# Kernel optimization log

Measured on AMD Instinct MI355X. Metric: run time of the kernel, lower is better.

## Reference

```python
import jax, jax.numpy as jnp
import numpy as np

H = 64           # edge/node/global hidden size
IN_F = 4         # node_attr_size
OUT_F = 1        # out_size
NUM_EMB = 100    # edge_num_embeddings
SKIP = True


def setup_inputs() -> dict:
    key = jax.random.key(0)
    ks = jax.random.split(key, 24)
    T, N, E = 4, 20000, 320000
    NNZ = 340000
    inp = {
        'node_attr': jax.random.normal(ks[0], (T, N, IN_F), jnp.float32),
        'global_attr': jax.random.normal(ks[1], (1, H), jnp.float32),
        'L_values': jax.random.normal(ks[2], (NNZ,), jnp.float32),
        'coeff': jnp.ones((1,), jnp.float32),
        'edge_attr': jax.random.randint(ks[3], (T, E), 0, NUM_EMB),
        'edge_index': jax.random.randint(ks[4], (2, E), 0, N),
        'L_index': jax.random.randint(ks[5], (2, NNZ), 0, N),
        'num_processing_steps': 4,
        # parameters
        'emb': jax.random.normal(ks[6], (NUM_EMB, H), jnp.float32) * 0.05,
        'W_ne': jax.random.normal(ks[7], (IN_F, H), jnp.float32) * 0.1,
        'b_ne': jnp.zeros((H,), jnp.float32),
        'W_eb': jax.random.normal(ks[8], ((H + 2 * H) * 2 + H, H), jnp.float32) * 0.05,
        'b_eb': jnp.zeros((H,), jnp.float32),
        'W_nb': jax.random.normal(ks[9], (2 * H + 2 * H + H, H), jnp.float32) * 0.05,
        'b_nb': jnp.zeros((H,), jnp.float32),
        'W_gb': jax.random.normal(ks[10], (H + H + H, H), jnp.float32) * 0.05,
        'b_gb': jnp.zeros((H,), jnp.float32),
        'W_d1': jax.random.normal(ks[11], (H, H), jnp.float32) * 0.1,
        'b_d1': jnp.zeros((H,), jnp.float32),
        'W_d2': jax.random.normal(ks[12], (H, OUT_F), jnp.float32) * 0.1,
        'b_d2': jnp.zeros((OUT_F,), jnp.float32),
        'W_i1': jax.random.normal(ks[13], (H, H), jnp.float32) * 0.1,
        'b_i1': jnp.zeros((H,), jnp.float32),
        'W_i2': jax.random.normal(ks[14], (H, IN_F), jnp.float32) * 0.1,
        'b_i2': jnp.zeros((IN_F,), jnp.float32),
    }
    return inp


def reference(node_attr, global_attr, L_values, coeff, emb, W_ne, b_ne,
              W_eb, b_eb, W_nb, b_nb, W_gb, b_gb, W_d1, b_d1, W_d2, b_d2,
              W_i1, b_i1, W_i2, b_i2, edge_attr, edge_index, L_index,
              num_processing_steps):
    T, N, _ = node_attr.shape
    s, r = edge_index[0], edge_index[1]
    Li, Lj = L_index[0], L_index[1]

    # encoders (all T steps at once)
    x_enc = jax.nn.relu(node_attr @ W_ne + b_ne)   # [T,N,H]
    e_enc = emb[edge_attr]                         # [T,E,H]

    def laplacian(h):  # sparse sp_L @ h, h: [N,H]
        return jax.ops.segment_sum(L_values[:, None] * h[Lj], Li, num_segments=N)

    def step(carry, xe):
        h_x, h_e, h_g = carry
        x_t, e_t = xe
        node_cat = jnp.concatenate([x_t, h_x], axis=-1)          # [N,2H]
        edge_cat = jnp.concatenate([e_t, h_e], axis=-1)          # [E,2H]
        g = h_g[0]                                               # [H]
        E_ = edge_cat.shape[0]
        # EdgeBlock: edges + sender + receiver + globals
        eb_in = jnp.concatenate([edge_cat, node_cat[s], node_cat[r],
                                 jnp.broadcast_to(g, (E_, g.shape[0]))], axis=-1)
        e_new = jax.nn.relu(eb_in @ W_eb + b_eb)                 # [E,H]
        # NodeBlock: scatter_add aggregates of received/sent edges
        recv = jax.ops.segment_sum(e_new, r, num_segments=N)
        sent = jax.ops.segment_sum(e_new, s, num_segments=N)
        nb_in = jnp.concatenate([recv, sent, node_cat,
                                 jnp.broadcast_to(g, (N, g.shape[0]))], axis=-1)
        x_new = jax.nn.relu(nb_in @ W_nb + b_nb)                 # [N,H]
        # GlobalBlock: scatter_mean (single graph -> mean)
        gb_in = jnp.concatenate([e_new.mean(0), x_new.mean(0), g])[None]
        g_new = jax.nn.relu(gb_in @ W_gb + b_gb)                 # [1,H]
        h_x_next = h_x + x_new if SKIP else x_new
        time_d = h_x_next - h_x
        spat_d = coeff[0] * laplacian(h_x_next)  # pde='diff': coeff * L u
        return (h_x_next, e_new, g_new), (h_x_next, time_d, spat_d)

    h0 = (jnp.zeros((N, H), jnp.float32),
          jnp.zeros((e_enc.shape[1], H), jnp.float32),
          global_attr)
    _, (hid, time_d, spat_d) = jax.lax.scan(step, h0, (x_enc, e_enc))

    # decoders over all steps
    out_nodes = jax.nn.relu(hid @ W_d1 + b_d1) @ W_d2 + b_d2     # [T,N,OUT_F]
    pred_in = jax.nn.relu(hid @ W_i1 + b_i1) @ W_i2 + b_i2       # [T,N,IN_F]
    return out_nodes, time_d, spat_d, pred_in
```

## Files before the change

### kernel.cpp

```cpp
#include <hip/hip_runtime.h>

#define TT 4
#define NN 20000
#define EE 320000
#define NZ 340000
#define NBKT 2500
#define SCB 2048
#define CNTB 2048

typedef __attribute__((ext_vector_type(8))) __bf16 bf16x8;
typedef __attribute__((ext_vector_type(16))) float f32x16;

__device__ __forceinline__ unsigned short f2bf(float f) {
    unsigned int u = __float_as_uint(f);
    u = (u + 0x7FFFu + ((u >> 16) & 1u)) >> 16;
    return (unsigned short)u;
}
__device__ __forceinline__ float bf2f(unsigned short h) {
    return __uint_as_float(((unsigned int)h) << 16);
}

#define GLL16(src, dst) __builtin_amdgcn_global_load_lds( \
    (const __attribute__((address_space(1))) unsigned int*)(src), \
    (__attribute__((address_space(3))) unsigned int*)(dst), 16, 0, 0)

#define XB (TT * NN / 4)

__global__ __launch_bounds__(256) void k_setup(
    const float* __restrict__ na, const float* __restrict__ W_ne,
    const float* __restrict__ b_ne, unsigned short* __restrict__ xenc,
    const int* __restrict__ r, const int* __restrict__ s,
    const int* __restrict__ Li, int* cnt_r, int* cnt_s, int* cnt_L,
    const float* __restrict__ W_eb, const float* __restrict__ W_nb,
    const float* __restrict__ W_d1, const float* __restrict__ W_i1,
    const float* __restrict__ emb, unsigned short* __restrict__ Bpe,
    unsigned short* __restrict__ Bpu, unsigned short* __restrict__ Bpn,
    unsigned short* __restrict__ Bpd, unsigned short* __restrict__ emb_bf) {
    int bid = blockIdx.x;
    if (bid < CNTB) {
        const int bucket = bid & 7;
        const int nlo = bucket * NBKT;
        const int cid = bid >> 3;
        const int stride = (CNTB >> 3) * 256;
        for (int i = cid * 256 + threadIdx.x; i < EE; i += stride) {
            int rv = r[i];
            if ((unsigned)(rv - nlo) < (unsigned)NBKT) atomicAdd(&cnt_r[rv], 1);
            int sv = s[i];
            if ((unsigned)(sv - nlo) < (unsigned)NBKT) atomicAdd(&cnt_s[sv], 1);
        }
        for (int i = cid * 256 + threadIdx.x; i < NZ; i += stride) {
            int lv = Li[i];
            if ((unsigned)(lv - nlo) < (unsigned)NBKT) atomicAdd(&cnt_L[lv], 1);
        }
        return;
    }
    bid -= CNTB;
    if (bid < 96) {
        int t = bid * 256 + threadIdx.x;
        if (t < 2 * 8 * 512) {
            int i = t & 7, l = (t >> 3) & 63, kb = (t >> 9) & 7, ch = t >> 12;
            int colv = ch * 32 + (l & 31);
            int k = kb * 16 + (l >> 5) * 8 + i;
            Bpe[t] = f2bf(W_eb[k * 64 + colv]);
        }
        if (t < 4 * 8 * 512) {
            int i = t & 7, l = (t >> 3) & 63, kb = (t >> 9) & 7, g = t >> 12;
            int colv = (g & 1) * 32 + (l & 31);
            int k = 128 + (g >> 1) * 128 + kb * 16 + (l >> 5) * 8 + i;
            Bpu[t] = f2bf(W_eb[k * 64 + colv]);
        }
        if (t < 2 * 16 * 512) {
            int i = t & 7, l = (t >> 3) & 63, kb = (t >> 9) % 16, ch = t / (16 * 512);
            int colv = ch * 32 + (l & 31);
            int k = kb * 16 + (l >> 5) * 8 + i;
            Bpn[t] = f2bf(W_nb[k * 64 + colv]);
        }
        if (t < 4 * 4 * 512) {
            int i = t & 7, l = (t >> 3) & 63, kb = (t >> 9) & 3, sec = t >> 11;
            int colv = (sec & 1) * 32 + (l & 31);
            int k = kb * 16 + (l >> 5) * 8 + i;
            const float* W = (sec < 2) ? W_d1 : W_i1;
            Bpd[t] = f2bf(W[k * 64 + colv]);
        }
        if (t < 100 * 64) emb_bf[t] = f2bf(emb[t]);
        return;
    }
    bid -= 96;
    int row = bid * 4 + (threadIdx.x >> 6);
    int j = threadIdx.x & 63;
    float4 a = *(const float4*)&na[(size_t)row * 4];
    float v = b_ne[j] + a.x * W_ne[j] + a.y * W_ne[64 + j] + a.z * W_ne[128 + j] + a.w * W_ne[192 + j];
    xenc[(size_t)row * 64 + j] = f2bf(fmaxf(v, 0.f));
}

__global__ __launch_bounds__(1024) void k_scan(int* cnt, int* rowp, int* wp) {
    int which = blockIdx.x;
    int* c = cnt + which * NN;
    int* row = rowp + which * (NN + 1);
    int* w = wp + which * NN;
    __shared__ int ssum[1024];
    int tid = threadIdx.x;
    const int CH = (NN + 1023) / 1024;
    int base = tid * CH;
    int s = 0;
    for (int i = 0; i < CH; ++i) { int idx = base + i; s += (idx < NN) ? c[idx] : 0; }
    ssum[tid] = s;
    __syncthreads();
    for (int o = 1; o < 1024; o <<= 1) {
        int v = (tid >= o) ? ssum[tid - o] : 0;
        __syncthreads();
        ssum[tid] += v;
        __syncthreads();
    }
    int run = (tid > 0) ? ssum[tid - 1] : 0;
    for (int i = 0; i < CH; ++i) {
        int idx = base + i;
        if (idx < NN) { row[idx] = run; w[idx] = run; run += c[idx]; }
    }
    if (tid == 1023) row[NN] = ssum[1023];
}

__global__ __launch_bounds__(64) void k_gbias(
    const float* __restrict__ W_gb, const float* __restrict__ b_gb,
    const float* __restrict__ W_eb, const float* __restrict__ b_eb,
    const float* __restrict__ W_nb, const float* __restrict__ b_nb,
    float* __restrict__ g_cur, float* __restrict__ e_sum, float* __restrict__ x_sum,
    float* __restrict__ gb_eb, float* __restrict__ gb_nb) {
    int j = threadIdx.x;
    float a = b_gb[j];
    for (int k = 0; k < 64; ++k) a += (e_sum[k] / (float)EE) * W_gb[k * 64 + j];
    for (int k = 0; k < 64; ++k) a += (x_sum[k] / (float)NN) * W_gb[(64 + k) * 64 + j];
    for (int k = 0; k < 64; ++k) a += g_cur[k] * W_gb[(128 + k) * 64 + j];
    float gv = fmaxf(a, 0.f);
    g_cur[j] = gv;
    e_sum[j] = 0.f;
    x_sum[j] = 0.f;
    float a1 = b_eb[j], a2 = b_nb[j];
    for (int k = 0; k < 64; ++k) {
        float gk = __shfl(gv, k, 64);
        a1 = fmaf(gk, W_eb[(384 + k) * 64 + j], a1);
        a2 = fmaf(gk, W_nb[(256 + k) * 64 + j], a2);
    }
    gb_eb[j] = a1;
    gb_nb[j] = a2;
}

__global__ __launch_bounds__(64) void k_usr(
    const unsigned short* __restrict__ xenc_t, const unsigned short* __restrict__ hx_bf,
    const unsigned short* __restrict__ Bpu, unsigned int* __restrict__ usr,
    const float* __restrict__ W_eb, const float* __restrict__ b_eb,
    const float* __restrict__ W_nb, const float* __restrict__ b_nb,
    float* __restrict__ g_cur, float* __restrict__ gb_eb, float* __restrict__ gb_nb) {
    const int ln = threadIdx.x;
    const int er = ln & 31, hi = ln >> 5;

    if (blockIdx.x == 0) {
        int j = ln;
        float gv = g_cur[j];
        float a1 = b_eb[j], a2 = b_nb[j];
        for (int k = 0; k < 64; ++k) {
            float gk = __shfl(gv, k, 64);
            a1 = fmaf(gk, W_eb[(384 + k) * 64 + j], a1);
            a2 = fmaf(gk, W_nb[(256 + k) * 64 + j], a2);
        }
        gb_eb[j] = a1;
        gb_nb[j] = a2;
    }

    const int n0 = blockIdx.x * 32;
    const int n = n0 + er;

    f32x16 a0, a1, a2, a3;
    #pragma unroll
    for (int i = 0; i < 16; ++i) { a0[i] = 0.f; a1[i] = 0.f; a2[i] = 0.f; a3[i] = 0.f; }

    const unsigned short* sx = xenc_t + (size_t)64 * n + hi * 8;
    const unsigned short* sh = hx_bf + (size_t)64 * n + hi * 8;
    #pragma unroll
    for (int c = 0; c < 2; ++c) {
        const unsigned short* src = c ? sh : sx;
        #pragma unroll
        for (int kb = 0; kb < 4; ++kb) {
            bf16x8 a = *(const bf16x8*)(src + kb * 16);
            int kg = c * 4 + kb;
            bf16x8 b0 = *(const bf16x8*)&Bpu[(size_t)((0 * 8 + kg) * 64 + ln) * 8];
            bf16x8 b1 = *(const bf16x8*)&Bpu[(size_t)((1 * 8 + kg) * 64 + ln) * 8];
            bf16x8 b2 = *(const bf16x8*)&Bpu[(size_t)((2 * 8 + kg) * 64 + ln) * 8];
            bf16x8 b3 = *(const bf16x8*)&Bpu[(size_t)((3 * 8 + kg) * 64 + ln) * 8];
            a0 = __builtin_amdgcn_mfma_f32_32x32x16_bf16(a, b0, a0, 0, 0, 0);
            a1 = __builtin_amdgcn_mfma_f32_32x32x16_bf16(a, b1, a1, 0, 0, 0);
            a2 = __builtin_amdgcn_mfma_f32_32x32x16_bf16(a, b2, a2, 0, 0, 0);
            a3 = __builtin_amdgcn_mfma_f32_32x32x16_bf16(a, b3, a3, 0, 0, 0);
        }
    }
    #pragma unroll
    for (int r = 0; r < 16; ++r) {
        int row = (r & 3) + 8 * (r >> 2) + 4 * hi;
        size_t o = (size_t)(n0 + row) * 64;
        usr[o + er]      = (unsigned int)f2bf(a0[r]) | ((unsigned int)f2bf(a1[r]) << 16);
        usr[o + 32 + er] = (unsigned int)f2bf(a2[r]) | ((unsigned int)f2bf(a3[r]) << 16);
    }
}

__global__ __launch_bounds__(512) void k_edge(
    int first, int scatterb, unsigned short* __restrict__ h_e,
    const unsigned short* __restrict__ emb_bf,
    const unsigned int* __restrict__ usr, const int* __restrict__ eattr_t,
    const int* __restrict__ sidx, const int* __restrict__ ridx,
    const unsigned short* __restrict__ Bp, const float* __restrict__ gbias,
    float* __restrict__ e_sum,
    const int* __restrict__ Li, const int* __restrict__ Lj,
    const float* __restrict__ Lv,
    int* wp_r, int* wp_s, int* wp_L,
    int* col_r, int* col_s, uint2* col_L8) {
    __shared__ unsigned short sBe[8192];
    __shared__ float sRed[8][64];
    const int tid = threadIdx.x;

    if ((int)blockIdx.x < scatterb) {
        const int sbid = blockIdx.x;
        const int bucket = sbid & 7;
        const int nlo = bucket * NBKT;
        const int cid = sbid >> 3;
        const int stride = (scatterb >> 3) * 512;
        for (int i = cid * 512 + tid; i < EE; i += stride) {
            int rv = ridx[i];
            if ((unsigned)(rv - nlo) < (unsigned)NBKT)
                col_r[atomicAdd(&wp_r[rv], 1)] = i;
            int sv = sidx[i];
            if ((unsigned)(sv - nlo) < (unsigned)NBKT)
                col_s[atomicAdd(&wp_s[sv], 1)] = i;
        }
        for (int i = cid * 512 + tid; i < NZ; i += stride) {
            int lv = Li[i];
            if ((unsigned)(lv - nlo) < (unsigned)NBKT) {
                int pos = atomicAdd(&wp_L[lv], 1);
                uint2 v;
                v.x = (unsigned int)Lj[i];
                v.y = __float_as_uint(Lv[i]);
                col_L8[pos] = v;
            }
        }
        return;
    }

    const int w = tid >> 6, ln = tid & 63;
    const int er = ln & 31, hi = ln >> 5;
    const int ebase = ((int)blockIdx.x - scatterb) * 256 + w * 32;
    const int e = ebase + er;

    const int siv = sidx[ebase + er];
    const int riv = ridx[ebase + er];
    const int ai = eattr_t[e];

    #pragma unroll
    for (int i = 0; i < 2; ++i) {
        int off = i * 4096 + w * 512;
        GLL16(Bp + off + ln * 8, sBe + off);
    }

    const unsigned short* s0 = emb_bf + (size_t)64 * ai + hi * 8;
    const unsigned short* s1 = h_e + (size_t)64 * e + hi * 8;
    bf16x8 a0 = *(const bf16x8*)(s0);
    bf16x8 a1 = *(const bf16x8*)(s0 + 16);
    bf16x8 a2 = *(const bf16x8*)(s0 + 32);
    bf16x8 a3 = *(const bf16x8*)(s0 + 48);
    bf16x8 a4{}, a5{}, a6{}, a7{};
    if (!first) {
        a4 = *(const bf16x8*)(s1);
        a5 = *(const bf16x8*)(s1 + 16);
        a6 = *(const bf16x8*)(s1 + 32);
        a7 = *(const bf16x8*)(s1 + 48);
    }

    f32x16 acc0, acc1;
    #pragma unroll
    for (int i = 0; i < 16; ++i) { acc0[i] = 0.f; acc1[i] = 0.f; }

    __syncthreads();

    #define EMM(AF, KG)                                                              \
        {                                                                            \
            bf16x8 b0 = *(const bf16x8*)&sBe[(((KG)) * 64 + ln) * 8];                \
            bf16x8 b1 = *(const bf16x8*)&sBe[((8 + (KG)) * 64 + ln) * 8];            \
            acc0 = __builtin_amdgcn_mfma_f32_32x32x16_bf16(AF, b0, acc0, 0, 0, 0);   \
            acc1 = __builtin_amdgcn_mfma_f32_32x32x16_bf16(AF, b1, acc1, 0, 0, 0);   \
        }
    EMM(a0, 0) EMM(a1, 1) EMM(a2, 2) EMM(a3, 3)
    if (!first) {
        EMM(a4, 4) EMM(a5, 5) EMM(a6, 6) EMM(a7, 7)
    }
    #undef EMM

    const float gb0 = gbias[er], gb1 = gbias[er + 32];
    float cs0 = 0.f, cs1 = 0.f;
    #pragma unroll
    for (int r = 0; r < 16; ++r) {
        int row = (r & 3) + 8 * (r >> 2) + 4 * hi;
        int si_row = __shfl(siv, row, 64);
        int ri_row = __shfl(riv, row, 64);
        unsigned int us = usr[(size_t)si_row * 64 + er];
        unsigned int ur = usr[(size_t)ri_row * 64 + 32 + er];
        size_t o = (size_t)(ebase + row) * 64;
        float v0 = fmaxf(acc0[r] + bf2f((unsigned short)(us & 0xFFFF))
                                 + bf2f((unsigned short)(ur & 0xFFFF)) + gb0, 0.f);
        float v1 = fmaxf(acc1[r] + bf2f((unsigned short)(us >> 16))
                                 + bf2f((unsigned short)(ur >> 16)) + gb1, 0.f);
        cs0 += v0; cs1 += v1;
        h_e[o + er] = f2bf(v0);
        h_e[o + er + 32] = f2bf(v1);
    }
    cs0 += __shfl_xor(cs0, 32, 64);
    cs1 += __shfl_xor(cs1, 32, 64);
    if (hi == 0) { sRed[w][er] = cs0; sRed[w][er + 32] = cs1; }
    __syncthreads();
    if (w == 0) {
        float t = 0.f;
        #pragma unroll
        for (int q = 0; q < 8; ++q) t += sRed[q][ln];
        atomicAdd(&e_sum[ln], t);
    }
}

__global__ __launch_bounds__(256) void k_glap(
    int gatherb,
    const unsigned short* __restrict__ h_e, const int* __restrict__ row_r,
    const int* __restrict__ col_r, const int* __restrict__ row_s,
    const int* __restrict__ col_s, unsigned short* __restrict__ recv,
    unsigned short* __restrict__ sentb,
    const unsigned short* __restrict__ hx_bf, const int* __restrict__ row_L,
    const uint2* __restrict__ col_L8, const float* __restrict__ coeff,
    float* __restrict__ spat_prev) {
    if ((int)blockIdx.x < gatherb) {
        int t = blockIdx.x * 256 + threadIdx.x;
        int sub = t & 63, n = t >> 6;
        int g = sub & 15, which = (sub >> 4) & 1, half = sub >> 5;
        const int* rowp = which ? row_s : row_r;
        const int* colp = which ? col_s : col_r;
        unsigned short* outp = which ? sentb : recv;

        float a0 = 0.f, a1 = 0.f, a2 = 0.f, a3 = 0.f;
        int b0 = rowp[n], b1 = rowp[n + 1];
        int mid = b0 + ((b1 - b0) >> 1);
        int p0 = half ? mid : b0;
        int p1 = half ? b1 : mid;
        for (int p = p0; p < p1; ++p) {
            uint2 v = *(const uint2*)&h_e[(size_t)64 * colp[p] + g * 4];
            a0 += bf2f((unsigned short)(v.x & 0xFFFF));
            a1 += bf2f((unsigned short)(v.x >> 16));
            a2 += bf2f((unsigned short)(v.y & 0xFFFF));
            a3 += bf2f((unsigned short)(v.y >> 16));
        }
        a0 += __shfl_xor(a0, 32, 64);
        a1 += __shfl_xor(a1, 32, 64);
        a2 += __shfl_xor(a2, 32, 64);
        a3 += __shfl_xor(a3, 32, 64);
        if (half == 0) {
            uint2 packed;
            packed.x = (unsigned int)f2bf(a0) | ((unsigned int)f2bf(a1) << 16);
            packed.y = (unsigned int)f2bf(a2) | ((unsigned int)f2bf(a3) << 16);
            *(uint2*)&outp[(size_t)64 * n + g * 4] = packed;
        }
        return;
    }
    int t = ((int)blockIdx.x - gatherb) * 256 + threadIdx.x;
    int sub = t & 31, n = t >> 5;
    int g = sub & 15, half = sub >> 4;
    float a0 = 0.f, a1 = 0.f, a2 = 0.f, a3 = 0.f;
    int b0 = row_L[n], b1 = row_L[n + 1];
    int mid = b0 + ((b1 - b0) >> 1);
    int p0 = half ? mid : b0;
    int p1 = half ? b1 : mid;
    for (int p = p0; p < p1; ++p) {
        uint2 e = col_L8[p];
        float lv = __uint_as_float(e.y);
        uint2 hv = *(const uint2*)&hx_bf[(size_t)64 * e.x + g * 4];
        a0 = fmaf(lv, bf2f((unsigned short)(hv.x & 0xFFFF)), a0);
        a1 = fmaf(lv, bf2f((unsigned short)(hv.x >> 16)), a1);
        a2 = fmaf(lv, bf2f((unsigned short)(hv.y & 0xFFFF)), a2);
        a3 = fmaf(lv, bf2f((unsigned short)(hv.y >> 16)), a3);
    }
    a0 += __shfl_xor(a0, 16, 64);
    a1 += __shfl_xor(a1, 16, 64);
    a2 += __shfl_xor(a2, 16, 64);
    a3 += __shfl_xor(a3, 16, 64);
    if (half == 0) {
        float c = coeff[0];
        float4 outv = {c * a0, c * a1, c * a2, c * a3};
        *(float4*)&spat_prev[(size_t)64 * n + g * 4] = outv;
    }
}

#define NODE_CHUNK(CIDX, BASE)                                                          \
    {                                                                                   \
        const unsigned short* src = (BASE) + hi * 8;                                    \
        _Pragma("unroll") for (int kb = 0; kb < 4; ++kb) {                              \
            bf16x8 a = *(const bf16x8*)(src + kb * 16);                                 \
            bf16x8 b0 = *(const bf16x8*)&Bp[(size_t)(((CIDX)*4 + kb) * 64 + ln) * 8];   \
            bf16x8 b1 = *(const bf16x8*)&Bp[(size_t)((16 + (CIDX)*4 + kb) * 64 + ln) * 8]; \
            acc0 = __builtin_amdgcn_mfma_f32_32x32x16_bf16(a, b0, acc0, 0, 0, 0);       \
            acc1 = __builtin_amdgcn_mfma_f32_32x32x16_bf16(a, b1, acc1, 0, 0, 0);       \
        }                                                                               \
    }

__global__ __launch_bounds__(64) void k_node(
    int has_next,
    const unsigned short* __restrict__ recv, const unsigned short* __restrict__ sentb,
    const unsigned short* __restrict__ xenc_t, float* __restrict__ h_x,
    unsigned short* __restrict__ hx_bf, const unsigned short* __restrict__ Bp,
    const float* __restrict__ gbias, float* __restrict__ x_sum,
    unsigned short* __restrict__ hid_t, float* __restrict__ timed_t,
    const unsigned short* __restrict__ xenc_next,
    const unsigned short* __restrict__ Bpu, unsigned int* __restrict__ usr) {
    __shared__ unsigned short sHx[32 * 64];
    const int ln = threadIdx.x;
    const int er = ln & 31, hi = ln >> 5;
    const int n0 = blockIdx.x * 32;
    const int n = n0 + er;

    f32x16 acc0, acc1;
    #pragma unroll
    for (int i = 0; i < 16; ++i) { acc0[i] = 0.f; acc1[i] = 0.f; }

    NODE_CHUNK(0, recv + (size_t)64 * n)
    NODE_CHUNK(1, sentb + (size_t)64 * n)
    NODE_CHUNK(2, xenc_t + (size_t)64 * n)
    NODE_CHUNK(3, hx_bf + (size_t)64 * n)

    const float gb0 = gbias[er], gb1 = gbias[er + 32];
    const int g0 = er >> 3, w0 = er & 7;
    float cs0 = 0.f, cs1 = 0.f;
    #pragma unroll
    for (int r = 0; r < 16; ++r) {
        int row = (r & 3) + 8 * (r >> 2) + 4 * hi;
        size_t o = (size_t)(n0 + row) * 64;
        float x0 = fmaxf(acc0[r] + gb0, 0.f);
        float x1 = fmaxf(acc1[r] + gb1, 0.f);
        cs0 += x0; cs1 += x1;
        float hx0 = h_x[o + er] + x0;
        float hx1 = h_x[o + er + 32] + x1;
        unsigned short hb0 = f2bf(hx0), hb1 = f2bf(hx1);
        h_x[o + er] = hx0;        h_x[o + er + 32] = hx1;
        hx_bf[o + er] = hb0;      hx_bf[o + er + 32] = hb1;
        hid_t[o + er] = hb0;      hid_t[o + er + 32] = hb1;
        timed_t[o + er] = x0;     timed_t[o + er + 32] = x1;
        int rs = row & 7;
        sHx[row * 64 + (((g0 ^ rs) << 3) | w0)] = hb0;
        sHx[row * 64 + ((((g0 + 4) ^ rs) << 3) | w0)] = hb1;
    }
    cs0 += __shfl_xor(cs0, 32, 64);
    cs1 += __shfl_xor(cs1, 32, 64);
    if (hi == 0) {
        atomicAdd(&x_sum[er], cs0);
        atomicAdd(&x_sum[er + 32], cs1);
    }
    if (!has_next) return;

    __syncthreads();

    f32x16 a0, a1, a2, a3;
    #pragma unroll
    for (int i = 0; i < 16; ++i) { a0[i] = 0.f; a1[i] = 0.f; a2[i] = 0.f; a3[i] = 0.f; }

    const unsigned short* sx = xenc_next + (size_t)64 * n + hi * 8;
    #pragma unroll
    for (int c = 0; c < 2; ++c) {
        #pragma unroll
        for (int kb = 0; kb < 4; ++kb) {
            bf16x8 a;
            if (c == 0) {
                a = *(const bf16x8*)(sx + kb * 16);
            } else {
                int gi = hi + 2 * kb;
                a = *(const bf16x8*)&sHx[er * 64 + ((gi ^ (er & 7)) << 3)];
            }
            int kg = c * 4 + kb;
            bf16x8 b0 = *(const bf16x8*)&Bpu[(size_t)((0 * 8 + kg) * 64 + ln) * 8];
            bf16x8 b1 = *(const bf16x8*)&Bpu[(size_t)((1 * 8 + kg) * 64 + ln) * 8];
            bf16x8 b2 = *(const bf16x8*)&Bpu[(size_t)((2 * 8 + kg) * 64 + ln) * 8];
            bf16x8 b3 = *(const bf16x8*)&Bpu[(size_t)((3 * 8 + kg) * 64 + ln) * 8];
            a0 = __builtin_amdgcn_mfma_f32_32x32x16_bf16(a, b0, a0, 0, 0, 0);
            a1 = __builtin_amdgcn_mfma_f32_32x32x16_bf16(a, b1, a1, 0, 0, 0);
            a2 = __builtin_amdgcn_mfma_f32_32x32x16_bf16(a, b2, a2, 0, 0, 0);
            a3 = __builtin_amdgcn_mfma_f32_32x32x16_bf16(a, b3, a3, 0, 0, 0);
        }
    }
    #pragma unroll
    for (int r = 0; r < 16; ++r) {
        int row = (r & 3) + 8 * (r >> 2) + 4 * hi;
        size_t o = (size_t)(n0 + row) * 64;
        usr[o + er]      = (unsigned int)f2bf(a0[r]) | ((unsigned int)f2bf(a1[r]) << 16);
        usr[o + 32 + er] = (unsigned int)f2bf(a2[r]) | ((unsigned int)f2bf(a3[r]) << 16);
    }
}

__global__ __launch_bounds__(256) void k_dec(
    const unsigned short* __restrict__ hid_bf, const unsigned short* __restrict__ Bpd,
    const float* __restrict__ b_d1, const float* __restrict__ W_d2,
    const float* __restrict__ b_d2, const float* __restrict__ b_i1,
    const float* __restrict__ W_i2, const float* __restrict__ b_i2,
    float* __restrict__ out_nodes, float* __restrict__ pred_in) {
    __shared__ unsigned short sDec[4][32 * 138];
    const int tid = threadIdx.x;
    const int w = tid >> 6, ln = tid & 63;
    const int er = ln & 31, hi = ln >> 5;
    const int row0 = (blockIdx.x * 4 + w) * 32;

    f32x16 ad0, ad1, ai0, ai1;
    #pragma unroll
    for (int i = 0; i < 16; ++i) { ad0[i] = 0.f; ad1[i] = 0.f; ai0[i] = 0.f; ai1[i] = 0.f; }

    const unsigned short* src = hid_bf + (size_t)(row0 + er) * 64 + hi * 8;
    #pragma unroll
    for (int kb = 0; kb < 4; ++kb) {
        bf16x8 a = *(const bf16x8*)(src + kb * 16);
        bf16x8 bd0 = *(const bf16x8*)&Bpd[((0 * 4 + kb) * 64 + ln) * 8];
        bf16x8 bd1 = *(const bf16x8*)&Bpd[((4 + kb) * 64 + ln) * 8];
        bf16x8 bi0 = *(const bf16x8*)&Bpd[((8 + kb) * 64 + ln) * 8];
        bf16x8 bi1 = *(const bf16x8*)&Bpd[((12 + kb) * 64 + ln) * 8];
        ad0 = __builtin_amdgcn_mfma_f32_32x32x16_bf16(a, bd0, ad0, 0, 0, 0);
        ad1 = __builtin_amdgcn_mfma_f32_32x32x16_bf16(a, bd1, ad1, 0, 0, 0);
        ai0 = __builtin_amdgcn_mfma_f32_32x32x16_bf16(a, bi0, ai0, 0, 0, 0);
        ai1 = __builtin_amdgcn_mfma_f32_32x32x16_bf16(a, bi1, ai1, 0, 0, 0);
    }

    const float bd0v = b_d1[er], bd1v = b_d1[er + 32];
    const float bi0v = b_i1[er], bi1v = b_i1[er + 32];
    unsigned short* sw = &sDec[w][0];
    #pragma unroll
    for (int r = 0; r < 16; ++r) {
        int row = (r & 3) + 8 * (r >> 2) + 4 * hi;
        sw[row * 138 + er]       = f2bf(fmaxf(ad0[r] + bd0v, 0.f));
        sw[row * 138 + er + 32]  = f2bf(fmaxf(ad1[r] + bd1v, 0.f));
        sw[row * 138 + er + 64]  = f2bf(fmaxf(ai0[r] + bi0v, 0.f));
        sw[row * 138 + er + 96]  = f2bf(fmaxf(ai1[r] + bi1v, 0.f));
    }
    __syncthreads();

    const int g_row = row0 + er;
    if (hi == 0) {
        float s = 0.f;
        for (int k = 0; k < 32; ++k) {
            unsigned int u = *(const unsigned int*)&sw[er * 138 + 2 * k];
            s = fmaf(bf2f((unsigned short)(u & 0xFFFF)), W_d2[2 * k], s);
            s = fmaf(bf2f((unsigned short)(u >> 16)), W_d2[2 * k + 1], s);
        }
        out_nodes[g_row] = s + b_d2[0];
    } else {
        float s0 = 0.f, s1 = 0.f, s2 = 0.f, s3 = 0.f;
        for (int k = 0; k < 32; ++k) {
            unsigned int u = *(const unsigned int*)&sw[er * 138 + 64 + 2 * k];
            float vlo = bf2f((unsigned short)(u & 0xFFFF));
            float vhi = bf2f((unsigned short)(u >> 16));
            float4 w0 = *(const float4*)&W_i2[(2 * k) * 4];
            float4 w1 = *(const float4*)&W_i2[(2 * k + 1) * 4];
            s0 = fmaf(vlo, w0.x, fmaf(vhi, w1.x, s0));
            s1 = fmaf(vlo, w0.y, fmaf(vhi, w1.y, s1));
            s2 = fmaf(vlo, w0.z, fmaf(vhi, w1.z, s2));
            s3 = fmaf(vlo, w0.w, fmaf(vhi, w1.w, s3));
        }
        float4 pv = {s0 + b_i2[0], s1 + b_i2[1], s2 + b_i2[2], s3 + b_i2[3]};
        *(float4*)&pred_in[(size_t)4 * g_row] = pv;
    }
}

extern "C" void kernel_launch(void* const* d_in, const int* in_sizes, int n_in,
                              void* d_out, int out_size, void* d_ws, size_t ws_size,
                              hipStream_t stream) {
    (void)in_sizes; (void)n_in; (void)out_size; (void)ws_size;
    const float* node_attr   = (const float*)d_in[0];
    const float* global_attr = (const float*)d_in[1];
    const float* L_values    = (const float*)d_in[2];
    const float* coeff       = (const float*)d_in[3];
    const int*   edge_attr   = (const int*)d_in[4];
    const int*   edge_index  = (const int*)d_in[5];
    const int*   L_index     = (const int*)d_in[6];
    const float* emb  = (const float*)d_in[8];
    const float* W_ne = (const float*)d_in[9];
    const float* b_ne = (const float*)d_in[10];
    const float* W_eb = (const float*)d_in[11];
    const float* b_eb = (const float*)d_in[12];
    const float* W_nb = (const float*)d_in[13];
    const float* b_nb = (const float*)d_in[14];
    const float* W_gb = (const float*)d_in[15];
    const float* b_gb = (const float*)d_in[16];
    const float* W_d1 = (const float*)d_in[17];
    const float* b_d1 = (const float*)d_in[18];
    const float* W_d2 = (const float*)d_in[19];
    const float* b_d2 = (const float*)d_in[20];
    const float* W_i1 = (const float*)d_in[21];
    const float* b_i1 = (const float*)d_in[22];
    const float* W_i2 = (const float*)d_in[23];
    const float* b_i2 = (const float*)d_in[24];

    const int* s_idx = edge_index;
    const int* r_idx = edge_index + EE;
    const int* Li = L_index;
    const int* Lj = L_index + NZ;

    char* ws = (char*)d_ws;
    size_t off = 0;
    auto alloc = [&](size_t bytes) -> void* {
        void* p = ws + off;
        off = (off + bytes + 255) & ~(size_t)255;
        return p;
    };
    unsigned short* xenc   = (unsigned short*)alloc((size_t)TT * NN * 64 * 2);
    unsigned short* hid    = (unsigned short*)alloc((size_t)TT * NN * 64 * 2);
    float*          h_x    = (float*)alloc((size_t)NN * 64 * 4);
    unsigned short* hx_bf  = (unsigned short*)alloc((size_t)NN * 64 * 2);
    unsigned short* h_e    = (unsigned short*)alloc((size_t)EE * 64 * 2);
    unsigned short* recv   = (unsigned short*)alloc((size_t)NN * 64 * 2);
    unsigned short* sentb  = (unsigned short*)alloc((size_t)NN * 64 * 2);
    unsigned int*   usr    = (unsigned int*)alloc((size_t)NN * 64 * 4);
    float* smalls          = (float*)alloc(2048);
    unsigned short* Bpe    = (unsigned short*)alloc((size_t)2 * 8 * 512 * 2);
    unsigned short* Bpu    = (unsigned short*)alloc((size_t)4 * 8 * 512 * 2);
    unsigned short* Bpn    = (unsigned short*)alloc((size_t)2 * 16 * 512 * 2);
    unsigned short* Bpd    = (unsigned short*)alloc((size_t)4 * 4 * 512 * 2);
    unsigned short* emb_bf = (unsigned short*)alloc((size_t)100 * 64 * 2);
    int* cnt    = (int*)alloc((size_t)3 * NN * 4);
    int* rowp   = (int*)alloc((size_t)3 * (NN + 1) * 4);
    int* wp     = (int*)alloc((size_t)3 * NN * 4);
    int* col_r  = (int*)alloc((size_t)EE * 4);
    int* col_s  = (int*)alloc((size_t)EE * 4);
    uint2* col_L8 = (uint2*)alloc((size_t)NZ * 8);

    float* g_cur = smalls;
    float* e_sum = smalls + 64;
    float* x_sum = smalls + 128;
    float* gb_eb = smalls + 192;
    float* gb_nb = smalls + 256;
    int* cnt_r = cnt, *cnt_s = cnt + NN, *cnt_L = cnt + 2 * NN;
    int* row_r = rowp, *row_s = rowp + (NN + 1), *row_L = rowp + 2 * (NN + 1);
    int* wp_r = wp, *wp_s = wp + NN, *wp_L = wp + 2 * NN;

    float* out_nodes = (float*)d_out;
    float* time_d = out_nodes + (size_t)TT * NN;
    float* spat_d = time_d + (size_t)TT * NN * 64;
    float* pred_in = spat_d + (size_t)TT * NN * 64;

    hipMemsetAsync(h_x, 0, (size_t)NN * 64 * 4, stream);
    hipMemsetAsync(hx_bf, 0, (size_t)NN * 64 * 2, stream);
    hipMemsetAsync(smalls, 0, 2048, stream);
    hipMemsetAsync(cnt, 0, (size_t)3 * NN * 4, stream);
    hipMemcpyAsync(g_cur, global_attr, 64 * 4, hipMemcpyDeviceToDevice, stream);

    k_setup<<<CNTB + 96 + XB, 256, 0, stream>>>(node_attr, W_ne, b_ne, xenc,
                                                r_idx, s_idx, Li, cnt_r, cnt_s, cnt_L,
                                                W_eb, W_nb, W_d1, W_i1, emb,
                                                Bpe, Bpu, Bpn, Bpd, emb_bf);
    k_scan<<<3, 1024, 0, stream>>>(cnt, rowp, wp);
    k_usr<<<NN / 32, 64, 0, stream>>>(xenc, hx_bf, Bpu, usr,
                                      W_eb, b_eb, W_nb, b_nb, g_cur, gb_eb, gb_nb);

    const int GBg = NN * 64 / 256;
    const int GBl = NN * 32 / 256;
    for (int t = 0; t < TT; ++t) {
        const unsigned short* xenc_t = xenc + (size_t)t * NN * 64;
        if (t > 0)
            k_gbias<<<1, 64, 0, stream>>>(W_gb, b_gb, W_eb, b_eb, W_nb, b_nb,
                                          g_cur, e_sum, x_sum, gb_eb, gb_nb);
        int scb = (t == 0) ? SCB : 0;
        k_edge<<<scb + EE / 256, 512, 0, stream>>>(
            t == 0, scb, h_e, emb_bf, usr,
            edge_attr + (size_t)t * EE, s_idx, r_idx, Bpe, gb_eb, e_sum,
            Li, Lj, L_values, wp_r, wp_s, wp_L, col_r, col_s, col_L8);
        int grid = GBg + ((t > 0) ? GBl : 0);
        float* spat_prev = spat_d + (size_t)((t > 0) ? t - 1 : 0) * NN * 64;
        k_glap<<<grid, 256, 0, stream>>>(GBg, h_e, row_r, col_r, row_s, col_s,
                                         recv, sentb, hx_bf, row_L, col_L8, coeff,
                                         spat_prev);
        const unsigned short* xenc_next =
            xenc + (size_t)((t < TT - 1) ? t + 1 : t) * NN * 64;
        k_node<<<NN / 32, 64, 0, stream>>>(t < TT - 1, recv, sentb, xenc_t, h_x, hx_bf,
                                           Bpn, gb_nb, x_sum,
                                           hid + (size_t)t * NN * 64,
                                           time_d + (size_t)t * NN * 64,
                                           xenc_next, Bpu, usr);
    }
    k_glap<<<GBl, 256, 0, stream>>>(0, h_e, row_r, col_r, row_s, col_s,
                                    recv, sentb, hx_bf, row_L, col_L8, coeff,
                                    spat_d + (size_t)(TT - 1) * NN * 64);
    k_dec<<<TT * NN / 128, 256, 0, stream>>>(hid, Bpd, b_d1, W_d2, b_d2,
                                             b_i1, W_i2, b_i2, out_nodes, pred_in);
}
```

Before: 627.3 us.

## Move Laplacian SpMV blocks from gather kernel into edge and decoder kernels

The Laplacian of the previous step's hidden state now runs as extra blocks inside the edge kernel rather than alongside the recv/sent gather. The last step's Laplacian is folded into the decoder launch, which removes one kernel launch. The intent is to overlap the memory-bound SpMV with the MFMA-heavy edge and decoder work instead of the equally memory-bound gather. The edge kernel uses 512-thread blocks, so its Laplacian slice is sized at 1250 blocks to cover all nodes, and it adds more parameters and register pressure to those kernels.

```diff
diff --git a/kernel.cpp b/kernel.cpp
--- a/kernel.cpp
+++ b/kernel.cpp
@@ -7,6 +7,8 @@
 #define NBKT 2500
 #define SCB 2048
 #define CNTB 2048
+#define LAPB_E 1250
+#define LAPB_D 2500
 
 typedef __attribute__((ext_vector_type(8))) __bf16 bf16x8;
 typedef __attribute__((ext_vector_type(16))) float f32x16;
@@ -23,6 +25,37 @@
 #define GLL16(src, dst) __builtin_amdgcn_global_load_lds( \
     (const __attribute__((address_space(1))) unsigned int*)(src), \
     (__attribute__((address_space(3))) unsigned int*)(dst), 16, 0, 0)
+
+__device__ __forceinline__ void lap_body(
+    int t, const unsigned short* __restrict__ hx_bf, const int* __restrict__ row_L,
+    const uint2* __restrict__ col_L8, const float* __restrict__ coeff,
+    float* __restrict__ spat) {
+    int sub = t & 31, n = t >> 5;
+    int g = sub & 15, half = sub >> 4;
+    float a0 = 0.f, a1 = 0.f, a2 = 0.f, a3 = 0.f;
+    int b0 = row_L[n], b1 = row_L[n + 1];
+    int mid = b0 + ((b1 - b0) >> 1);
+    int p0 = half ? mid : b0;
+    int p1 = half ? b1 : mid;
+    for (int p = p0; p < p1; ++p) {
+        uint2 e = col_L8[p];
+        float lv = __uint_as_float(e.y);
+        uint2 hv = *(const uint2*)&hx_bf[(size_t)64 * e.x + g * 4];
+        a0 = fmaf(lv, bf2f((unsigned short)(hv.x & 0xFFFF)), a0);
+        a1 = fmaf(lv, bf2f((unsigned short)(hv.x >> 16)), a1);
+        a2 = fmaf(lv, bf2f((unsigned short)(hv.y & 0xFFFF)), a2);
+        a3 = fmaf(lv, bf2f((unsigned short)(hv.y >> 16)), a3);
+    }
+    a0 += __shfl_xor(a0, 16, 64);
+    a1 += __shfl_xor(a1, 16, 64);
+    a2 += __shfl_xor(a2, 16, 64);
+    a3 += __shfl_xor(a3, 16, 64);
+    if (half == 0) {
+        float c = coeff[0];
+        float4 outv = {c * a0, c * a1, c * a2, c * a3};
+        *(float4*)&spat[(size_t)64 * n + g * 4] = outv;
+    }
+}
 
 #define XB (TT * NN / 4)
 
@@ -203,7 +236,7 @@
 }
 
 __global__ __launch_bounds__(512) void k_edge(
-    int first, int scatterb, unsigned short* __restrict__ h_e,
+    int first, int scatterb, int lapb, unsigned short* __restrict__ h_e,
     const unsigned short* __restrict__ emb_bf,
     const unsigned int* __restrict__ usr, const int* __restrict__ eattr_t,
     const int* __restrict__ sidx, const int* __restrict__ ridx,
@@ -212,7 +245,10 @@
     const int* __restrict__ Li, const int* __restrict__ Lj,
     const float* __restrict__ Lv,
     int* wp_r, int* wp_s, int* wp_L,
-    int* col_r, int* col_s, uint2* col_L8) {
+    int* col_r, int* col_s, uint2* col_L8,
+    const unsigned short* __restrict__ hx_bf, const int* __restrict__ row_L,
+    const uint2* __restrict__ col_L8c, const float* __restrict__ coeff,
+    float* __restrict__ spat_prev) {
     __shared__ unsigned short sBe[8192];
     __shared__ float sRed[8][64];
     const int tid = threadIdx.x;
@@ -243,10 +279,15 @@
         }
         return;
     }
+    if ((int)blockIdx.x < scatterb + lapb) {
+        int t = ((int)blockIdx.x - scatterb) * 512 + tid;
+        lap_body(t, hx_bf, row_L, col_L8c, coeff, spat_prev);
+        return;
+    }
 
     const int w = tid >> 6, ln = tid & 63;
     const int er = ln & 31, hi = ln >> 5;
-    const int ebase = ((int)blockIdx.x - scatterb) * 256 + w * 32;
+    const int ebase = ((int)blockIdx.x - scatterb - lapb) * 256 + w * 32;
     const int e = ebase + er;
 
     const int siv = sidx[ebase + er];
@@ -322,72 +363,39 @@
     }
 }
 
-__global__ __launch_bounds__(256) void k_glap(
-    int gatherb,
+__global__ __launch_bounds__(256) void k_gather(
     const unsigned short* __restrict__ h_e, const int* __restrict__ row_r,
     const int* __restrict__ col_r, const int* __restrict__ row_s,
     const int* __restrict__ col_s, unsigned short* __restrict__ recv,
-    unsigned short* __restrict__ sentb,
-    const unsigned short* __restrict__ hx_bf, const int* __restrict__ row_L,
-    const uint2* __restrict__ col_L8, const float* __restrict__ coeff,
-    float* __restrict__ spat_prev) {
-    if ((int)blockIdx.x < gatherb) {
-        int t = blockIdx.x * 256 + threadIdx.x;
-        int sub = t & 63, n = t >> 6;
-        int g = sub & 15, which = (sub >> 4) & 1, half = sub >> 5;
-        const int* rowp = which ? row_s : row_r;
-        const int* colp = which ? col_s : col_r;
-        unsigned short* outp = which ? sentb : recv;
-
-        float a0 = 0.f, a1 = 0.f, a2 = 0.f, a3 = 0.f;
-        int b0 = rowp[n], b1 = rowp[n + 1];
-        int mid = b0 + ((b1 - b0) >> 1);
-        int p0 = half ? mid : b0;
-        int p1 = half ? b1 : mid;
-        for (int p = p0; p < p1; ++p) {
-            uint2 v = *(const uint2*)&h_e[(size_t)64 * colp[p] + g * 4];
-            a0 += bf2f((unsigned short)(v.x & 0xFFFF));
-            a1 += bf2f((unsigned short)(v.x >> 16));
-            a2 += bf2f((unsigned short)(v.y & 0xFFFF));
-            a3 += bf2f((unsigned short)(v.y >> 16));
-        }
-        a0 += __shfl_xor(a0, 32, 64);
-        a1 += __shfl_xor(a1, 32, 64);
-        a2 += __shfl_xor(a2, 32, 64);
-        a3 += __shfl_xor(a3, 32, 64);
-        if (half == 0) {
-            uint2 packed;
-            packed.x = (unsigned int)f2bf(a0) | ((unsigned int)f2bf(a1) << 16);
-            packed.y = (unsigned int)f2bf(a2) | ((unsigned int)f2bf(a3) << 16);
-            *(uint2*)&outp[(size_t)64 * n + g * 4] = packed;
-        }
-        return;
-    }
-    int t = ((int)blockIdx.x - gatherb) * 256 + threadIdx.x;
-    int sub = t & 31, n = t >> 5;
-    int g = sub & 15, half = sub >> 4;
+    unsigned short* __restrict__ sentb) {
+    int t = blockIdx.x * 256 + threadIdx.x;
+    int sub = t & 63, n = t >> 6;
+    int g = sub & 15, which = (sub >> 4) & 1, half = sub >> 5;
+    const int* rowp = which ? row_s : row_r;
+    const int* colp = which ? col_s : col_r;
+    unsigned short* outp = which ? sentb : recv;
+
     float a0 = 0.f, a1 = 0.f, a2 = 0.f, a3 = 0.f;
-    int b0 = row_L[n], b1 = row_L[n + 1];
+    int b0 = rowp[n], b1 = rowp[n + 1];
     int mid = b0 + ((b1 - b0) >> 1);
     int p0 = half ? mid : b0;
     int p1 = half ? b1 : mid;
     for (int p = p0; p < p1; ++p) {
-        uint2 e = col_L8[p];
-        float lv = __uint_as_float(e.y);
-        uint2 hv = *(const uint2*)&hx_bf[(size_t)64 * e.x + g * 4];
-        a0 = fmaf(lv, bf2f((unsigned short)(hv.x & 0xFFFF)), a0);
-        a1 = fmaf(lv, bf2f((unsigned short)(hv.x >> 16)), a1);
-        a2 = fmaf(lv, bf2f((unsigned short)(hv.y & 0xFFFF)), a2);
-        a3 = fmaf(lv, bf2f((unsigned short)(hv.y >> 16)), a3);
-    }
-    a0 += __shfl_xor(a0, 16, 64);
-    a1 += __shfl_xor(a1, 16, 64);
-    a2 += __shfl_xor(a2, 16, 64);
-    a3 += __shfl_xor(a3, 16, 64);
+        uint2 v = *(const uint2*)&h_e[(size_t)64 * colp[p] + g * 4];
+        a0 += bf2f((unsigned short)(v.x & 0xFFFF));
+        a1 += bf2f((unsigned short)(v.x >> 16));
+        a2 += bf2f((unsigned short)(v.y & 0xFFFF));
+        a3 += bf2f((unsigned short)(v.y >> 16));
+    }
+    a0 += __shfl_xor(a0, 32, 64);
+    a1 += __shfl_xor(a1, 32, 64);
+    a2 += __shfl_xor(a2, 32, 64);
+    a3 += __shfl_xor(a3, 32, 64);
     if (half == 0) {
-        float c = coeff[0];
-        float4 outv = {c * a0, c * a1, c * a2, c * a3};
-        *(float4*)&spat_prev[(size_t)64 * n + g * 4] = outv;
+        uint2 packed;
+        packed.x = (unsigned int)f2bf(a0) | ((unsigned int)f2bf(a1) << 16);
+        packed.y = (unsigned int)f2bf(a2) | ((unsigned int)f2bf(a3) << 16);
+        *(uint2*)&outp[(size_t)64 * n + g * 4] = packed;
     }
 }
 
@@ -495,16 +503,27 @@
 }
 
 __global__ __launch_bounds__(256) void k_dec(
+    int lapb,
     const unsigned short* __restrict__ hid_bf, const unsigned short* __restrict__ Bpd,
     const float* __restrict__ b_d1, const float* __restrict__ W_d2,
     const float* __restrict__ b_d2, const float* __restrict__ b_i1,
     const float* __restrict__ W_i2, const float* __restrict__ b_i2,
-    float* __restrict__ out_nodes, float* __restrict__ pred_in) {
+    float* __restrict__ out_nodes, float* __restrict__ pred_in,
+    const unsigned short* __restrict__ hx_bf, const int* __restrict__ row_L,
+    const uint2* __restrict__ col_L8, const float* __restrict__ coeff,
+    float* __restrict__ spat_last) {
     __shared__ unsigned short sDec[4][32 * 138];
     const int tid = threadIdx.x;
+
+    if ((int)blockIdx.x < lapb) {
+        int t = blockIdx.x * 256 + tid;
+        lap_body(t, hx_bf, row_L, col_L8, coeff, spat_last);
+        return;
+    }
+
     const int w = tid >> 6, ln = tid & 63;
     const int er = ln & 31, hi = ln >> 5;
-    const int row0 = (blockIdx.x * 4 + w) * 32;
+    const int row0 = (((int)blockIdx.x - lapb) * 4 + w) * 32;
 
     f32x16 ad0, ad1, ai0, ai1;
     #pragma unroll
@@ -655,22 +674,21 @@
                                       W_eb, b_eb, W_nb, b_nb, g_cur, gb_eb, gb_nb);
 
     const int GBg = NN * 64 / 256;
-    const int GBl = NN * 32 / 256;
     for (int t = 0; t < TT; ++t) {
         const unsigned short* xenc_t = xenc + (size_t)t * NN * 64;
         if (t > 0)
             k_gbias<<<1, 64, 0, stream>>>(W_gb, b_gb, W_eb, b_eb, W_nb, b_nb,
                                           g_cur, e_sum, x_sum, gb_eb, gb_nb);
         int scb = (t == 0) ? SCB : 0;
-        k_edge<<<scb + EE / 256, 512, 0, stream>>>(
-            t == 0, scb, h_e, emb_bf, usr,
+        int lapb = (t > 0) ? LAPB_E : 0;
+        float* spat_prev = spat_d + (size_t)((t > 0) ? t - 1 : 0) * NN * 64;
+        k_edge<<<scb + lapb + EE / 256, 512, 0, stream>>>(
+            t == 0, scb, lapb, h_e, emb_bf, usr,
             edge_attr + (size_t)t * EE, s_idx, r_idx, Bpe, gb_eb, e_sum,
-            Li, Lj, L_values, wp_r, wp_s, wp_L, col_r, col_s, col_L8);
-        int grid = GBg + ((t > 0) ? GBl : 0);
-        float* spat_prev = spat_d + (size_t)((t > 0) ? t - 1 : 0) * NN * 64;
-        k_glap<<<grid, 256, 0, stream>>>(GBg, h_e, row_r, col_r, row_s, col_s,
-                                         recv, sentb, hx_bf, row_L, col_L8, coeff,
-                                         spat_prev);
+            Li, Lj, L_values, wp_r, wp_s, wp_L, col_r, col_s, col_L8,
+            hx_bf, row_L, col_L8, coeff, spat_prev);
+        k_gather<<<GBg, 256, 0, stream>>>(h_e, row_r, col_r, row_s, col_s,
+                                          recv, sentb);
         const unsigned short* xenc_next =
             xenc + (size_t)((t < TT - 1) ? t + 1 : t) * NN * 64;
         k_node<<<NN / 32, 64, 0, stream>>>(t < TT - 1, recv, sentb, xenc_t, h_x, hx_bf,
@@ -679,9 +697,7 @@
                                            time_d + (size_t)t * NN * 64,
                                            xenc_next, Bpu, usr);
     }
-    k_glap<<<GBl, 256, 0, stream>>>(0, h_e, row_r, col_r, row_s, col_s,
-                                    recv, sentb, hx_bf, row_L, col_L8, coeff,
-                                    spat_d + (size_t)(TT - 1) * NN * 64);
-    k_dec<<<TT * NN / 128, 256, 0, stream>>>(hid, Bpd, b_d1, W_d2, b_d2,
-                                             b_i1, W_i2, b_i2, out_nodes, pred_in);
-}
+    k_dec<<<LAPB_D + TT * NN / 128, 256, 0, stream>>>(
+        LAPB_D, hid, Bpd, b_d1, W_d2, b_d2, b_i1, W_i2, b_i2, out_nodes, pred_in,
+        hx_bf, row_L, col_L8, coeff, spat_d + (size_t)(TT - 1) * NN * 64);
+}
```

Result: no change. 634.5 us (+1.2%).

## Permute edges into receiver-sorted order and merge scatter build with usr kernel

Applied to the files above, without the earlier changes.

Edges are renumbered into receiver-CSR order during the CSR build, so per-edge sender, receiver and attribute arrays are stored permuted. The receiver aggregation then reads h_e contiguously, and the sender aggregation goes through a precomputed col_s2r indirection. The scatter build moves out of the first k_edge launch into a combined kernel alongside the usr GEMM, and the first k_edge launch now performs the col_s2r fixup instead. This removes the random gather for receive sums at the cost of extra index arrays and a permutation pass over edge attributes.

```diff
diff --git a/kernel.cpp b/kernel.cpp
--- a/kernel.cpp
+++ b/kernel.cpp
@@ -145,16 +145,58 @@
     gb_nb[j] = a2;
 }
 
-__global__ __launch_bounds__(64) void k_usr(
-    const unsigned short* __restrict__ xenc_t, const unsigned short* __restrict__ hx_bf,
+__global__ __launch_bounds__(256) void k_susr(
+    int scatterb, int nusr,
+    const int* __restrict__ sidx, const int* __restrict__ ridx,
+    const int* __restrict__ Li, const int* __restrict__ Lj,
+    const float* __restrict__ Lv, const int* __restrict__ edge_attr,
+    int* wp_r, int* wp_s, int* wp_L,
+    int* __restrict__ rpos, int* __restrict__ sp, int* __restrict__ rp,
+    int* __restrict__ ap, int* __restrict__ col_s, uint2* __restrict__ col_L8,
+    const unsigned short* __restrict__ xenc0, const unsigned short* __restrict__ hx_bf,
     const unsigned short* __restrict__ Bpu, unsigned int* __restrict__ usr,
     const float* __restrict__ W_eb, const float* __restrict__ b_eb,
     const float* __restrict__ W_nb, const float* __restrict__ b_nb,
     float* __restrict__ g_cur, float* __restrict__ gb_eb, float* __restrict__ gb_nb) {
-    const int ln = threadIdx.x;
+    const int tid = threadIdx.x;
+    if ((int)blockIdx.x < scatterb) {
+        const int bucket = blockIdx.x & 7;
+        const int nlo = bucket * NBKT;
+        const int cid = blockIdx.x >> 3;
+        const int stride = (scatterb >> 3) * 256;
+        for (int i = cid * 256 + tid; i < EE; i += stride) {
+            int rv = ridx[i];
+            int sv = sidx[i];
+            if ((unsigned)(rv - nlo) < (unsigned)NBKT) {
+                int pos = atomicAdd(&wp_r[rv], 1);
+                rpos[i] = pos;
+                sp[pos] = sv;
+                rp[pos] = rv;
+                ap[pos] = edge_attr[i];
+                ap[EE + pos] = edge_attr[EE + i];
+                ap[2 * EE + pos] = edge_attr[2 * EE + i];
+                ap[3 * EE + pos] = edge_attr[3 * EE + i];
+            }
+            if ((unsigned)(sv - nlo) < (unsigned)NBKT)
+                col_s[atomicAdd(&wp_s[sv], 1)] = i;
+        }
+        for (int i = cid * 256 + tid; i < NZ; i += stride) {
+            int lv = Li[i];
+            if ((unsigned)(lv - nlo) < (unsigned)NBKT) {
+                int pos = atomicAdd(&wp_L[lv], 1);
+                uint2 v;
+                v.x = (unsigned int)Lj[i];
+                v.y = __float_as_uint(Lv[i]);
+                col_L8[pos] = v;
+            }
+        }
+        return;
+    }
+    const int ln = tid & 63;
+    const int wid = ((int)blockIdx.x - scatterb) * 4 + (tid >> 6);
     const int er = ln & 31, hi = ln >> 5;
 
-    if (blockIdx.x == 0) {
+    if (wid == 0) {
         int j = ln;
         float gv = g_cur[j];
         float a1 = b_eb[j], a2 = b_nb[j];
@@ -166,15 +208,16 @@
         gb_eb[j] = a1;
         gb_nb[j] = a2;
     }
-
-    const int n0 = blockIdx.x * 32;
+    if (wid >= nusr) return;
+
+    const int n0 = wid * 32;
     const int n = n0 + er;
 
     f32x16 a0, a1, a2, a3;
     #pragma unroll
     for (int i = 0; i < 16; ++i) { a0[i] = 0.f; a1[i] = 0.f; a2[i] = 0.f; a3[i] = 0.f; }
 
-    const unsigned short* sx = xenc_t + (size_t)64 * n + hi * 8;
+    const unsigned short* sx = xenc0 + (size_t)64 * n + hi * 8;
     const unsigned short* sh = hx_bf + (size_t)64 * n + hi * 8;
     #pragma unroll
     for (int c = 0; c < 2; ++c) {
@@ -203,55 +246,32 @@
 }
 
 __global__ __launch_bounds__(512) void k_edge(
-    int first, int scatterb, unsigned short* __restrict__ h_e,
+    int first, int fixb, unsigned short* __restrict__ h_e,
     const unsigned short* __restrict__ emb_bf,
-    const unsigned int* __restrict__ usr, const int* __restrict__ eattr_t,
-    const int* __restrict__ sidx, const int* __restrict__ ridx,
+    const unsigned int* __restrict__ usr, const int* __restrict__ ap_t,
+    const int* __restrict__ sp, const int* __restrict__ rp,
     const unsigned short* __restrict__ Bp, const float* __restrict__ gbias,
     float* __restrict__ e_sum,
-    const int* __restrict__ Li, const int* __restrict__ Lj,
-    const float* __restrict__ Lv,
-    int* wp_r, int* wp_s, int* wp_L,
-    int* col_r, int* col_s, uint2* col_L8) {
+    const int* __restrict__ col_s, const int* __restrict__ rpos,
+    int* __restrict__ col_s2r) {
     __shared__ unsigned short sBe[8192];
     __shared__ float sRed[8][64];
     const int tid = threadIdx.x;
 
-    if ((int)blockIdx.x < scatterb) {
-        const int sbid = blockIdx.x;
-        const int bucket = sbid & 7;
-        const int nlo = bucket * NBKT;
-        const int cid = sbid >> 3;
-        const int stride = (scatterb >> 3) * 512;
-        for (int i = cid * 512 + tid; i < EE; i += stride) {
-            int rv = ridx[i];
-            if ((unsigned)(rv - nlo) < (unsigned)NBKT)
-                col_r[atomicAdd(&wp_r[rv], 1)] = i;
-            int sv = sidx[i];
-            if ((unsigned)(sv - nlo) < (unsigned)NBKT)
-                col_s[atomicAdd(&wp_s[sv], 1)] = i;
-        }
-        for (int i = cid * 512 + tid; i < NZ; i += stride) {
-            int lv = Li[i];
-            if ((unsigned)(lv - nlo) < (unsigned)NBKT) {
-                int pos = atomicAdd(&wp_L[lv], 1);
-                uint2 v;
-                v.x = (unsigned int)Lj[i];
-                v.y = __float_as_uint(Lv[i]);
-                col_L8[pos] = v;
-            }
-        }
+    if ((int)blockIdx.x < fixb) {
+        int p = blockIdx.x * 512 + tid;
+        col_s2r[p] = rpos[col_s[p]];
         return;
     }
 
     const int w = tid >> 6, ln = tid & 63;
     const int er = ln & 31, hi = ln >> 5;
-    const int ebase = ((int)blockIdx.x - scatterb) * 256 + w * 32;
+    const int ebase = ((int)blockIdx.x - fixb) * 256 + w * 32;
     const int e = ebase + er;
 
-    const int siv = sidx[ebase + er];
-    const int riv = ridx[ebase + er];
-    const int ai = eattr_t[e];
+    const int siv = sp[e];
+    const int riv = rp[e];
+    const int ai = ap_t[e];
 
     #pragma unroll
     for (int i = 0; i < 2; ++i) {
@@ -325,9 +345,8 @@
 __global__ __launch_bounds__(256) void k_glap(
     int gatherb,
     const unsigned short* __restrict__ h_e, const int* __restrict__ row_r,
-    const int* __restrict__ col_r, const int* __restrict__ row_s,
-    const int* __restrict__ col_s, unsigned short* __restrict__ recv,
-    unsigned short* __restrict__ sentb,
+    const int* __restrict__ row_s, const int* __restrict__ col_s2r,
+    unsigned short* __restrict__ recv, unsigned short* __restrict__ sentb,
     const unsigned short* __restrict__ hx_bf, const int* __restrict__ row_L,
     const uint2* __restrict__ col_L8, const float* __restrict__ coeff,
     float* __restrict__ spat_prev) {
@@ -336,7 +355,6 @@
         int sub = t & 63, n = t >> 6;
         int g = sub & 15, which = (sub >> 4) & 1, half = sub >> 5;
         const int* rowp = which ? row_s : row_r;
-        const int* colp = which ? col_s : col_r;
         unsigned short* outp = which ? sentb : recv;
 
         float a0 = 0.f, a1 = 0.f, a2 = 0.f, a3 = 0.f;
@@ -344,12 +362,23 @@
         int mid = b0 + ((b1 - b0) >> 1);
         int p0 = half ? mid : b0;
         int p1 = half ? b1 : mid;
-        for (int p = p0; p < p1; ++p) {
-            uint2 v = *(const uint2*)&h_e[(size_t)64 * colp[p] + g * 4];
-            a0 += bf2f((unsigned short)(v.x & 0xFFFF));
-            a1 += bf2f((unsigned short)(v.x >> 16));
-            a2 += bf2f((unsigned short)(v.y & 0xFFFF));
-            a3 += bf2f((unsigned short)(v.y >> 16));
+        if (which == 0) {
+            for (int p = p0; p < p1; ++p) {
+                uint2 v = *(const uint2*)&h_e[(size_t)64 * p + g * 4];
+                a0 += bf2f((unsigned short)(v.x & 0xFFFF));
+                a1 += bf2f((unsigned short)(v.x >> 16));
+                a2 += bf2f((unsigned short)(v.y & 0xFFFF));
+                a3 += bf2f((unsigned short)(v.y >> 16));
+            }
+        } else {
+            for (int p = p0; p < p1; ++p) {
+                int r2 = col_s2r[p];
+                uint2 v = *(const uint2*)&h_e[(size_t)64 * r2 + g * 4];
+                a0 += bf2f((unsigned short)(v.x & 0xFFFF));
+                a1 += bf2f((unsigned short)(v.x >> 16));
+                a2 += bf2f((unsigned short)(v.y & 0xFFFF));
+                a3 += bf2f((unsigned short)(v.y >> 16));
+            }
         }
         a0 += __shfl_xor(a0, 32, 64);
         a1 += __shfl_xor(a1, 32, 64);
@@ -619,11 +648,15 @@
     unsigned short* Bpn    = (unsigned short*)alloc((size_t)2 * 16 * 512 * 2);
     unsigned short* Bpd    = (unsigned short*)alloc((size_t)4 * 4 * 512 * 2);
     unsigned short* emb_bf = (unsigned short*)alloc((size_t)100 * 64 * 2);
-    int* cnt    = (int*)alloc((size_t)3 * NN * 4);
-    int* rowp   = (int*)alloc((size_t)3 * (NN + 1) * 4);
-    int* wp     = (int*)alloc((size_t)3 * NN * 4);
-    int* col_r  = (int*)alloc((size_t)EE * 4);
-    int* col_s  = (int*)alloc((size_t)EE * 4);
+    int* cnt     = (int*)alloc((size_t)3 * NN * 4);
+    int* rowp    = (int*)alloc((size_t)3 * (NN + 1) * 4);
+    int* wp      = (int*)alloc((size_t)3 * NN * 4);
+    int* col_s   = (int*)alloc((size_t)EE * 4);
+    int* rpos    = (int*)alloc((size_t)EE * 4);
+    int* sp      = (int*)alloc((size_t)EE * 4);
+    int* rp      = (int*)alloc((size_t)EE * 4);
+    int* ap      = (int*)alloc((size_t)4 * EE * 4);
+    int* col_s2r = (int*)alloc((size_t)EE * 4);
     uint2* col_L8 = (uint2*)alloc((size_t)NZ * 8);
 
     float* g_cur = smalls;
@@ -651,8 +684,15 @@
                                                 W_eb, W_nb, W_d1, W_i1, emb,
                                                 Bpe, Bpu, Bpn, Bpd, emb_bf);
     k_scan<<<3, 1024, 0, stream>>>(cnt, rowp, wp);
-    k_usr<<<NN / 32, 64, 0, stream>>>(xenc, hx_bf, Bpu, usr,
-                                      W_eb, b_eb, W_nb, b_nb, g_cur, gb_eb, gb_nb);
+    const int NUSR = NN / 32;
+    const int USRB = (NUSR + 3) / 4;
+    k_susr<<<SCB + USRB, 256, 0, stream>>>(SCB, NUSR,
+                                           s_idx, r_idx, Li, Lj, L_values, edge_attr,
+                                           wp_r, wp_s, wp_L,
+                                           rpos, sp, rp, ap, col_s, col_L8,
+                                           xenc, hx_bf, Bpu, usr,
+                                           W_eb, b_eb, W_nb, b_nb,
+                                           g_cur, gb_eb, gb_nb);
 
     const int GBg = NN * 64 / 256;
     const int GBl = NN * 32 / 256;
@@ -661,14 +701,13 @@
         if (t > 0)
             k_gbias<<<1, 64, 0, stream>>>(W_gb, b_gb, W_eb, b_eb, W_nb, b_nb,
                                           g_cur, e_sum, x_sum, gb_eb, gb_nb);
-        int scb = (t == 0) ? SCB : 0;
-        k_edge<<<scb + EE / 256, 512, 0, stream>>>(
-            t == 0, scb, h_e, emb_bf, usr,
-            edge_attr + (size_t)t * EE, s_idx, r_idx, Bpe, gb_eb, e_sum,
-            Li, Lj, L_values, wp_r, wp_s, wp_L, col_r, col_s, col_L8);
+        int fixb = (t == 0) ? EE / 512 : 0;
+        k_edge<<<fixb + EE / 256, 512, 0, stream>>>(
+            t == 0, fixb, h_e, emb_bf, usr, ap + (size_t)t * EE, sp, rp,
+            Bpe, gb_eb, e_sum, col_s, rpos, col_s2r);
         int grid = GBg + ((t > 0) ? GBl : 0);
         float* spat_prev = spat_d + (size_t)((t > 0) ? t - 1 : 0) * NN * 64;
-        k_glap<<<grid, 256, 0, stream>>>(GBg, h_e, row_r, col_r, row_s, col_s,
+        k_glap<<<grid, 256, 0, stream>>>(GBg, h_e, row_r, row_s, col_s2r,
                                          recv, sentb, hx_bf, row_L, col_L8, coeff,
                                          spat_prev);
         const unsigned short* xenc_next =
@@ -679,7 +718,7 @@
                                            time_d + (size_t)t * NN * 64,
                                            xenc_next, Bpu, usr);
     }
-    k_glap<<<GBl, 256, 0, stream>>>(0, h_e, row_r, col_r, row_s, col_s,
+    k_glap<<<GBl, 256, 0, stream>>>(0, h_e, row_r, row_s, col_s2r,
                                     recv, sentb, hx_bf, row_L, col_L8, coeff,
                                     spat_d + (size_t)(TT - 1) * NN * 64);
     k_dec<<<TT * NN / 128, 256, 0, stream>>>(hid, Bpd, b_d1, W_d2, b_d2,
```

Measured after the change: 657.3 us. +4.8%, slower.
